# Kernel optimization log

Hardware: AMD Instinct MI355X
Metric: run time of the kernel (lower is better)

## Reference

```python
import jax, jax.numpy as jnp
import numpy as np

N_LAYERS = 12
N_CH = 256
N_IN = 4
KS = 3
SPECT_CH = 640


def conv1d(x, w, b, dilation):
    # x: [B, T, Cin], w: [K, Cin, Cout] (WIO), SAME padding, given dilation
    y = jax.lax.conv_general_dilated(
        x, w, window_strides=(1,), padding='SAME',
        rhs_dilation=(dilation,), dimension_numbers=('NWC', 'WIO', 'NWC'))
    return y + b


def setup_inputs() -> dict:
    key = jax.random.key(0)
    ks = jax.random.split(key, 16)
    s = 0.02
    inp = {}
    inp['audio'] = jax.random.normal(ks[0], (8, 4096, N_IN), dtype=jnp.float32)
    inp['spect'] = jax.random.normal(ks[1], (8, 4096, SPECT_CH), dtype=jnp.float32)
    # start 1x1 conv: [Cin, Cout]
    inp['w_start'] = jax.random.normal(ks[2], (N_IN, N_CH), dtype=jnp.float32) * s
    inp['b_start'] = jnp.zeros((N_CH,), dtype=jnp.float32)
    # dilated in_layers: stacked [L, K, Cin, 2*Cout]
    inp['w_in'] = jax.random.normal(ks[3], (N_LAYERS, KS, N_CH, 2 * N_CH), dtype=jnp.float32) * s
    inp['b_in'] = jnp.zeros((N_LAYERS, 2 * N_CH), dtype=jnp.float32)
    # cond 1x1 convs: stacked [L, SPECT_CH, 2*Cout]
    inp['w_cond'] = jax.random.normal(ks[4], (N_LAYERS, SPECT_CH, 2 * N_CH), dtype=jnp.float32) * s
    inp['b_cond'] = jnp.zeros((N_LAYERS, 2 * N_CH), dtype=jnp.float32)
    # res_skip 1x1 convs: first L-1 have 2*Cout, last has Cout
    inp['w_res'] = jax.random.normal(ks[5], (N_LAYERS - 1, N_CH, 2 * N_CH), dtype=jnp.float32) * s
    inp['b_res'] = jnp.zeros((N_LAYERS - 1, 2 * N_CH), dtype=jnp.float32)
    inp['w_res_last'] = jax.random.normal(ks[6], (N_CH, N_CH), dtype=jnp.float32) * s
    inp['b_res_last'] = jnp.zeros((N_CH,), dtype=jnp.float32)
    # end 1x1 conv (zero-initialized in the original; use small random for a
    # non-degenerate numerical baseline)
    inp['w_end'] = jax.random.normal(ks[7], (N_CH, 2 * N_IN), dtype=jnp.float32) * s
    inp['b_end'] = jnp.zeros((2 * N_IN,), dtype=jnp.float32)
    return inp


def reference(audio, spect, w_start, b_start, w_in, b_in, w_cond, b_cond,
              w_res, b_res, w_res_last, b_res_last, w_end, b_end):
    # start: 1x1 conv == matmul over channels
    started = jnp.einsum('btc,cd->btd', audio, w_start) + b_start  # [B,T,256]
    # precompute all conditioning projections: [L,B,T,512]
    cond_all = jnp.einsum('btc,lcd->lbtd', spect, w_cond) + b_cond[:, None, None, :]
    output = None
    for i in range(N_LAYERS):
        in_l = conv1d(started, w_in[i], b_in[i], 2 ** i)  # [B,T,512]
        acts = in_l + cond_all[i]
        half_tanh = jnp.tanh(acts[..., :N_CH])
        half_sig = jax.nn.sigmoid(acts[..., N_CH:])
        activated = half_tanh * half_sig  # [B,T,256]
        if i < N_LAYERS - 1:
            rs = jnp.einsum('btc,cd->btd', activated, w_res[i]) + b_res[i]
            started = started + rs[..., :N_CH]
            skip = rs[..., N_CH:]
        else:
            skip = jnp.einsum('btc,cd->btd', activated, w_res_last) + b_res_last
        output = skip if output is None else output + skip
    out = jnp.einsum('btc,cd->btd', output, w_end) + b_end  # [B,T,2*N_IN]
    return out
```

## Files before the change

kernel.cpp:

```cpp
#include <hip/hip_runtime.h>
#include <cstdint>

#define PAD 2048
#define KG 1408

typedef float f32x4 __attribute__((ext_vector_type(4)));
typedef __bf16 bf16x8 __attribute__((ext_vector_type(8)));
typedef __bf16 bf16x4 __attribute__((ext_vector_type(4)));

__device__ __forceinline__ void g2l16(const void* g, void* l) {
    __builtin_amdgcn_global_load_lds(
        (__attribute__((address_space(1))) void*)(uintptr_t)g,
        (__attribute__((address_space(3))) void*)(uint32_t)(uintptr_t)l,
        16, 0, 0);
}


__global__ void cvt_bf16_kernel(const float4* __restrict__ src, bf16x4* __restrict__ dst, int n4) {
    int idx = blockIdx.x * 256 + threadIdx.x;
    if (idx < n4) {
        float4 v = src[idx];
        bf16x4 o = {(__bf16)v.x, (__bf16)v.y, (__bf16)v.z, (__bf16)v.w};
        dst[idx] = o;
    }
}

__global__ void init_started_kernel(const float* __restrict__ audio, const float* __restrict__ w_start,
                                    const float* __restrict__ b_start, __bf16* __restrict__ started_pad) {
    int pr = blockIdx.x * 4 + (threadIdx.x >> 6);
    int c0 = (threadIdx.x & 63) * 4;
    int off = pr & 8191;
    bf16x4 o = {(__bf16)0.f, (__bf16)0.f, (__bf16)0.f, (__bf16)0.f};
    if (off >= PAD && off < PAD + 4096) {
        int r = ((pr >> 13) << 12) + (off - PAD);
        float a0 = audio[r * 4 + 0], a1 = audio[r * 4 + 1], a2 = audio[r * 4 + 2], a3 = audio[r * 4 + 3];
        for (int j = 0; j < 4; ++j) {
            int c = c0 + j;
            o[j] = (__bf16)(b_start[c] + a0 * w_start[c] + a1 * w_start[256 + c]
                            + a2 * w_start[512 + c] + a3 * w_start[768 + c]);
        }
    }
    *(bf16x4*)&started_pad[(size_t)pr * 256 + c0] = o;
}

__global__ void transpose_gate(const float* __restrict__ w_in, const float* __restrict__ w_cond,
                               __bf16* __restrict__ Wg) {
    __shared__ float tile[64][65];
    int i = blockIdx.z;
    int k0 = blockIdx.y * 64, n0 = blockIdx.x * 64;
    int tid = threadIdx.x, c = tid & 63, rr = tid >> 6;
    for (int it = 0; it < 16; ++it) {
        int kl = it * 4 + rr;
        int k = k0 + kl;
        int np = n0 + c;
        int phys = ((np >> 4) & 1) * 256 + (np >> 5) * 16 + (np & 15);
        float v;
        if (k < 768) v = w_in[((i * 3 + (k >> 8)) * 256 + (k & 255)) * 512 + phys];
        else         v = w_cond[(i * 640 + (k - 768)) * 512 + phys];
        tile[kl][c] = v;
    }
    __syncthreads();
    for (int it = 0; it < 16; ++it) {
        int nl = it * 4 + rr;
        Wg[(size_t)(i * 512 + n0 + nl) * KG + k0 + c] = (__bf16)tile[c][nl];
    }
}

__global__ void transpose_kn(const float* __restrict__ src, __bf16* __restrict__ dst,
                             int K, int N, int srcLS, int dstLS) {
    __shared__ float tile[64][65];
    int i = blockIdx.z;
    int k0 = blockIdx.y * 64, n0 = blockIdx.x * 64;
    int tid = threadIdx.x, c = tid & 63, rr = tid >> 6;
    const float* s = src + (size_t)i * srcLS;
    __bf16* dp = dst + (size_t)i * dstLS;
    for (int it = 0; it < 16; ++it) {
        int kl = it * 4 + rr;
        tile[kl][c] = s[(k0 + kl) * N + n0 + c];
    }
    __syncthreads();
    for (int it = 0; it < 16; ++it) {
        int nl = it * 4 + rr;
        dp[(size_t)(n0 + nl) * K + k0 + c] = (__bf16)tile[c][nl];
    }
}

__global__ void bias_gate_kernel(const float* __restrict__ b_in, const float* __restrict__ b_cond,
                                 float* __restrict__ bias) {
    int idx = blockIdx.x * 256 + threadIdx.x;
    int i = idx >> 9, np = idx & 511;
    int phys = ((np >> 4) & 1) * 256 + (np >> 5) * 16 + (np & 15);
    bias[idx] = b_in[i * 512 + phys] + b_cond[i * 512 + phys];
}

__global__ void wfold_kernel(const float* __restrict__ w_res, const float* __restrict__ w_res_last,
                             const float* __restrict__ w_end, const float* __restrict__ b_res,
                             const float* __restrict__ b_res_last, const float* __restrict__ b_end,
                             float* __restrict__ wfold, float* __restrict__ outconst) {
    if (blockIdx.x == 96) {
        __shared__ float red[256][8];
        int j = threadIdx.x;
        float bsum = b_res_last[j];
        for (int i = 0; i < 11; ++i) bsum += b_res[i * 512 + 256 + j];
        for (int c = 0; c < 8; ++c) red[j][c] = bsum * w_end[j * 8 + c];
        __syncthreads();
        if (j < 8) {
            float s = b_end[j];
            for (int t = 0; t < 256; ++t) s += red[t][j];
            outconst[j] = s;
        }
        return;
    }
    int idx = blockIdx.x * 256 + threadIdx.x;
    int i = idx >> 11, rem = idx & 2047, k = rem >> 3, c = rem & 7;
    float s = 0.f;
    if (i < 11) {
        const float* wr = w_res + (size_t)(i * 256 + k) * 512 + 256;
        for (int j = 0; j < 256; ++j) s += wr[j] * w_end[j * 8 + c];
    } else {
        const float* wr = w_res_last + k * 256;
        for (int j = 0; j < 256; ++j) s += wr[j] * w_end[j * 8 + c];
    }
    wfold[idx] = s;
}


__global__ __launch_bounds__(256, 2) void gate_kernel(
    const __bf16* __restrict__ started_pad, const __bf16* __restrict__ spect,
    const __bf16* __restrict__ Wg,
    const float* __restrict__ bias,
    __bf16* __restrict__ activated, int d) {
    __shared__ __align__(16) __bf16 SMEM[24576];
    const int tid = threadIdx.x;
    const int m0 = blockIdx.x * 128;
    const int n0 = blockIdx.y * 256;
    const int padbase = ((m0 >> 12) << 13) + PAD + (m0 & 4095);
    const int srow = tid >> 2;
    const int skq = (tid & 3) * 8;
    const int wave = tid >> 6, lane = tid & 63;
    const int wm = (wave >> 1) * 64, wn = (wave & 1) * 128;
    const int quad = lane >> 4, l15 = lane & 15;

    f32x4 acc[4][8];
    for (int i = 0; i < 4; i++)
        for (int j = 0; j < 8; j++) acc[i][j] = f32x4{0.f, 0.f, 0.f, 0.f};

    const __bf16* Bbase = Wg + (n0 + srow) * KG + skq;

    bf16x8 rA[2], rB[4];
    auto loadTile = [&](int kk) {
        const __bf16* gA0;
        int rstride;
        if (kk < 768) {
            int tap = kk >> 8;
            int koff = kk & 255;
            gA0 = started_pad + (padbase + srow + (tap - 1) * d) * 256 + koff + skq;
            rstride = 256;
        } else {
            gA0 = spect + (m0 + srow) * 640 + (kk - 768) + skq;
            rstride = 640;
        }
        rA[0] = *(const bf16x8*)gA0;
        rA[1] = *(const bf16x8*)(gA0 + 64 * rstride);
        const __bf16* gB0 = Bbase + kk;
        rB[0] = *(const bf16x8*)gB0;
        rB[1] = *(const bf16x8*)(gB0 + 64 * KG);
        rB[2] = *(const bf16x8*)(gB0 + 128 * KG);
        rB[3] = *(const bf16x8*)(gB0 + 192 * KG);
    };
    auto stash = [&](int buf) {
        __bf16* Ab = SMEM + buf * 4096;
        __bf16* Bb = SMEM + 8192 + buf * 8192;
        *(bf16x8*)&Ab[srow * 32 + skq] = rA[0];
        *(bf16x8*)&Ab[(64 + srow) * 32 + skq] = rA[1];
        *(bf16x8*)&Bb[srow * 32 + skq] = rB[0];
        *(bf16x8*)&Bb[(64 + srow) * 32 + skq] = rB[1];
        *(bf16x8*)&Bb[(128 + srow) * 32 + skq] = rB[2];
        *(bf16x8*)&Bb[(192 + srow) * 32 + skq] = rB[3];
    };

    loadTile(0);
    stash(0);
    loadTile(32);
    __syncthreads();

    for (int ks = 0; ks < 44; ++ks) {
        const int cur = ks & 1, nxt = cur ^ 1;
        const __bf16* Ab = SMEM + cur * 4096;
        const __bf16* Bb = SMEM + 8192 + cur * 8192;
        bf16x8 a[4], b[8];
        for (int mi = 0; mi < 4; mi++) a[mi] = *(const bf16x8*)&Ab[(wm + mi * 16 + l15) * 32 + quad * 8];
        for (int ni = 0; ni < 8; ni++) b[ni] = *(const bf16x8*)&Bb[(wn + ni * 16 + l15) * 32 + quad * 8];
        if (ks + 1 < 44) stash(nxt);
        if (ks + 2 < 44) loadTile((ks + 2) * 32);
        for (int mi = 0; mi < 4; mi++)
            for (int ni = 0; ni < 8; ni++)
                acc[mi][ni] = __builtin_amdgcn_mfma_f32_16x16x32_bf16(a[mi], b[ni], acc[mi][ni], 0, 0, 0);
        __syncthreads();
    }

    __bf16* tile = SMEM;
    for (int nj = 0; nj < 4; ++nj) {
        int colT = wn + nj * 32 + l15;
        float bt = bias[n0 + colT];
        float bs = bias[n0 + colT + 16];
        int chl = (wn >> 1) + nj * 16 + l15;
        for (int mi = 0; mi < 4; ++mi) {
            for (int reg = 0; reg < 4; ++reg) {
                int row = wm + mi * 16 + quad * 4 + reg;
                float xt = acc[mi][2 * nj][reg] + bt;
                float xs = acc[mi][2 * nj + 1][reg] + bs;
                float th = 2.f / (1.f + __expf(-2.f * xt)) - 1.f;
                float sg = 1.f / (1.f + __expf(-xs));
                tile[row * 132 + chl] = (__bf16)(th * sg);
            }
        }
    }
    __syncthreads();
    int chb = n0 >> 1;
    for (int pass = 0; pass < 8; ++pass) {
        int row = (tid >> 4) + 16 * pass;
        int seg = tid & 15;
        bf16x8 v = *(const bf16x8*)&tile[row * 132 + seg * 8];
        *(bf16x8*)&activated[(m0 + row) * 256 + chb + seg * 8] = v;
    }
}

__global__ __launch_bounds__(256) void res_kernel(
    const __bf16* __restrict__ activated, const __bf16* __restrict__ Wr,
    const float* __restrict__ b_res,
    const float* __restrict__ wfold,
    const float* __restrict__ outconst,
    __bf16* __restrict__ started_pad, float* __restrict__ out, int initOut) {
    __shared__ __align__(16) __bf16 As[128 * 32];
    __shared__ __align__(16) __bf16 Bs[128 * 32];
    __shared__ __align__(16) __bf16 WfB[16 * 264];
    const int tid = threadIdx.x;
    const int m0 = blockIdx.x * 128;
    const int n0 = blockIdx.y * 128;
    const int srow = tid >> 2;
    const int skq = (tid & 3) * 8;
    const int wave = tid >> 6, lane = tid & 63;
    const int wm = (wave >> 1) * 64, wn = (wave & 1) * 64;
    const int quad = lane >> 4, l15 = lane & 15;
    const bool doOut = (blockIdx.y == 0);
    const bool outWave = doOut && (wn == 0);

    f32x4 acc[4][4];
    for (int i = 0; i < 4; i++)
        for (int j = 0; j < 4; j++) acc[i][j] = f32x4{0.f, 0.f, 0.f, 0.f};
    f32x4 acc_o[4];
    for (int i = 0; i < 4; i++) acc_o[i] = f32x4{0.f, 0.f, 0.f, 0.f};

    const __bf16* Abase = activated + (m0 + srow) * 256 + skq;
    const __bf16* Bbase = Wr + (n0 + srow) * 256 + skq;

    if (doOut) {
        for (int t = 0; t < 16; ++t) {
            int e = t * 256 + tid;
            int col = e >> 8, k = e & 255;
            WfB[col * 264 + k] = (col < 8) ? (__bf16)wfold[k * 8 + col] : (__bf16)0.f;
        }
    }

    for (int ks = 0; ks < 8; ++ks) {
        int kk = ks * 32;
        g2l16(Abase + kk, &As[srow * 32 + skq]);
        g2l16(Abase + kk + 64 * 256, &As[(64 + srow) * 32 + skq]);
        g2l16(Bbase + kk, &Bs[srow * 32 + skq]);
        g2l16(Bbase + kk + 64 * 256, &Bs[(64 + srow) * 32 + skq]);
        __syncthreads();
        bf16x8 a[4], b[4];
        for (int mi = 0; mi < 4; mi++) a[mi] = *(const bf16x8*)&As[(wm + mi * 16 + l15) * 32 + quad * 8];
        for (int ni = 0; ni < 4; ni++) b[ni] = *(const bf16x8*)&Bs[(wn + ni * 16 + l15) * 32 + quad * 8];
        for (int mi = 0; mi < 4; mi++)
            for (int ni = 0; ni < 4; ni++)
                acc[mi][ni] = __builtin_amdgcn_mfma_f32_16x16x32_bf16(a[mi], b[ni], acc[mi][ni], 0, 0, 0);
        if (outWave) {
            bf16x8 bx = *(const bf16x8*)&WfB[l15 * 264 + kk + quad * 8];
            for (int mi = 0; mi < 4; mi++)
                acc_o[mi] = __builtin_amdgcn_mfma_f32_16x16x32_bf16(a[mi], bx, acc_o[mi], 0, 0, 0);
        }
        __syncthreads();
    }

    for (int ni = 0; ni < 4; ++ni) {
        int col = n0 + wn + ni * 16 + l15;
        float bcol = b_res[col];
        for (int mi = 0; mi < 4; ++mi) {
            for (int reg = 0; reg < 4; ++reg) {
                int r = m0 + wm + mi * 16 + quad * 4 + reg;
                int pr = ((r >> 12) << 13) + PAD + (r & 4095);
                int idx = pr * 256 + col;
                float f = (float)started_pad[idx] + acc[mi][ni][reg] + bcol;
                started_pad[idx] = (__bf16)f;
            }
        }
    }
    if (outWave && l15 < 8) {
        for (int mi = 0; mi < 4; ++mi) {
            for (int reg = 0; reg < 4; ++reg) {
                int r = m0 + wm + mi * 16 + quad * 4 + reg;
                float base = initOut ? outconst[l15] : out[r * 8 + l15];
                out[r * 8 + l15] = base + acc_o[mi][reg];
            }
        }
    }
}

__global__ __launch_bounds__(256) void outacc_kernel(
    const __bf16* __restrict__ activated, const float* __restrict__ wfold,
    float* __restrict__ out) {
    __shared__ __align__(16) float Wf[2048];
    int tid = threadIdx.x;
    ((float4*)Wf)[tid] = ((const float4*)wfold)[tid];
    ((float4*)Wf)[256 + tid] = ((const float4*)wfold)[256 + tid];
    __syncthreads();
    int row2 = tid >> 1, half = tid & 1;
    int r = blockIdx.x * 128 + row2;
    const bf16x8* ap = (const bf16x8*)(activated + r * 256);
    const float4* wf = (const float4*)Wf;
    float ox = 0.f, oy = 0.f, oz = 0.f, ow = 0.f;
    for (int c8 = 0; c8 < 32; ++c8) {
        bf16x8 av = ap[c8];
        for (int e = 0; e < 8; ++e) {
            float a = (float)av[e];
            float4 w = wf[(c8 * 8 + e) * 2 + half];
            ox += a * w.x; oy += a * w.y; oz += a * w.z; ow += a * w.w;
        }
    }
    float4* op = (float4*)&out[r * 8 + half * 4];
    float4 o = *op;
    o.x += ox; o.y += oy; o.z += oz; o.w += ow;
    *op = o;
}


extern "C" void kernel_launch(void* const* d_in, const int* in_sizes, int n_in,
                              void* d_out, int out_size, void* d_ws, size_t ws_size,
                              hipStream_t stream) {
    const float* audio      = (const float*)d_in[0];
    const float* spect      = (const float*)d_in[1];
    const float* w_start    = (const float*)d_in[2];
    const float* b_start    = (const float*)d_in[3];
    const float* w_in       = (const float*)d_in[4];
    const float* b_in       = (const float*)d_in[5];
    const float* w_cond     = (const float*)d_in[6];
    const float* b_cond     = (const float*)d_in[7];
    const float* w_res      = (const float*)d_in[8];
    const float* b_res      = (const float*)d_in[9];
    const float* w_res_last = (const float*)d_in[10];
    const float* b_res_last = (const float*)d_in[11];
    const float* w_end      = (const float*)d_in[12];
    const float* b_end      = (const float*)d_in[13];
    float* out = (float*)d_out;

    char* ws = (char*)d_ws;
    __bf16* started_pad = (__bf16*)ws; ws += 33554432;
    __bf16* activated   = (__bf16*)ws; ws += 16777216;
    __bf16* spect_bf    = (__bf16*)ws; ws += 41943040;
    __bf16* Wg          = (__bf16*)ws; ws += 17301504;
    __bf16* Wr          = (__bf16*)ws; ws += 1441792;
    float*  wfold       = (float*)ws;  ws += 98304;
    float*  biasg       = (float*)ws;  ws += 24576;
    float*  outconst    = (float*)ws;  ws += 256;

    init_started_kernel<<<dim3(16384), 256, 0, stream>>>(audio, w_start, b_start, started_pad);
    cvt_bf16_kernel<<<dim3(20480), 256, 0, stream>>>((const float4*)spect, (bf16x4*)spect_bf, 5242880);
    transpose_gate<<<dim3(8, 22, 12), 256, 0, stream>>>(w_in, w_cond, Wg);
    transpose_kn<<<dim3(4, 4, 11), 256, 0, stream>>>(w_res, Wr, 256, 512, 256 * 512, 256 * 256);
    bias_gate_kernel<<<dim3(24), 256, 0, stream>>>(b_in, b_cond, biasg);
    wfold_kernel<<<dim3(97), 256, 0, stream>>>(w_res, w_res_last, w_end, b_res, b_res_last, b_end,
                                               wfold, outconst);

    for (int i = 0; i < 12; ++i) {
        gate_kernel<<<dim3(256, 2), 256, 0, stream>>>(
            started_pad, spect_bf, Wg + (size_t)i * 512 * KG, biasg + i * 512, activated, 1 << i);
        if (i < 11) {
            res_kernel<<<dim3(256, 2), 256, 0, stream>>>(
                activated, Wr + (size_t)i * 256 * 256, b_res + i * 512,
                wfold + i * 2048, outconst, started_pad, out, i == 0 ? 1 : 0);
        } else {
            outacc_kernel<<<dim3(256), 256, 0, stream>>>(activated, wfold + 11 * 2048, out);
        }
    }
}
```

Measured before the change: 1.106 ms.

## Use direct global-to-LDS loads with XOR-swizzled LDS layout in gate and res GEMMs

Result: no change. 1.096 ms (-0.9%).

```diff
diff --git a/kernel.cpp b/kernel.cpp
--- a/kernel.cpp
+++ b/kernel.cpp
@@ -135,77 +135,79 @@
     const int m0 = blockIdx.x * 128;
     const int n0 = blockIdx.y * 256;
     const int padbase = ((m0 >> 12) << 13) + PAD + (m0 & 4095);
-    const int srow = tid >> 2;
-    const int skq = (tid & 3) * 8;
     const int wave = tid >> 6, lane = tid & 63;
     const int wm = (wave >> 1) * 64, wn = (wave & 1) * 128;
     const int quad = lane >> 4, l15 = lane & 15;
 
+    const int srow = tid >> 2;
+    const int swcol = ((tid & 3) ^ (srow & 3)) * 8;
+
     f32x4 acc[4][8];
+    #pragma unroll
     for (int i = 0; i < 4; i++)
+        #pragma unroll
         for (int j = 0; j < 8; j++) acc[i][j] = f32x4{0.f, 0.f, 0.f, 0.f};
 
-    const __bf16* Bbase = Wg + (n0 + srow) * KG + skq;
-
-    bf16x8 rA[2], rB[4];
-    auto loadTile = [&](int kk) {
-        const __bf16* gA0;
-        int rstride;
+    auto stage = [&](int kk, int s) {
+        __bf16* Ad = SMEM + s * 4096 + tid * 8;
+        const __bf16* gA;
+        int rs;
         if (kk < 768) {
             int tap = kk >> 8;
             int koff = kk & 255;
-            gA0 = started_pad + (padbase + srow + (tap - 1) * d) * 256 + koff + skq;
-            rstride = 256;
+            gA = started_pad + (size_t)(padbase + srow + (tap - 1) * d) * 256 + koff + swcol;
+            rs = 256;
         } else {
-            gA0 = spect + (m0 + srow) * 640 + (kk - 768) + skq;
-            rstride = 640;
-        }
-        rA[0] = *(const bf16x8*)gA0;
-        rA[1] = *(const bf16x8*)(gA0 + 64 * rstride);
-        const __bf16* gB0 = Bbase + kk;
-        rB[0] = *(const bf16x8*)gB0;
-        rB[1] = *(const bf16x8*)(gB0 + 64 * KG);
-        rB[2] = *(const bf16x8*)(gB0 + 128 * KG);
-        rB[3] = *(const bf16x8*)(gB0 + 192 * KG);
+            gA = spect + (size_t)(m0 + srow) * 640 + (kk - 768) + swcol;
+            rs = 640;
+        }
+        g2l16(gA, Ad);
+        g2l16(gA + 64 * rs, Ad + 2048);
+        const __bf16* gB = Wg + (size_t)(n0 + srow) * KG + kk + swcol;
+        __bf16* Bd = SMEM + 8192 + s * 8192 + tid * 8;
+        g2l16(gB, Bd);
+        g2l16(gB + 64 * KG, Bd + 2048);
+        g2l16(gB + 128 * KG, Bd + 4096);
+        g2l16(gB + 192 * KG, Bd + 6144);
     };
-    auto stash = [&](int buf) {
-        __bf16* Ab = SMEM + buf * 4096;
-        __bf16* Bb = SMEM + 8192 + buf * 8192;
-        *(bf16x8*)&Ab[srow * 32 + skq] = rA[0];
-        *(bf16x8*)&Ab[(64 + srow) * 32 + skq] = rA[1];
-        *(bf16x8*)&Bb[srow * 32 + skq] = rB[0];
-        *(bf16x8*)&Bb[(64 + srow) * 32 + skq] = rB[1];
-        *(bf16x8*)&Bb[(128 + srow) * 32 + skq] = rB[2];
-        *(bf16x8*)&Bb[(192 + srow) * 32 + skq] = rB[3];
-    };
-
-    loadTile(0);
-    stash(0);
-    loadTile(32);
+
+    stage(0, 0);
     __syncthreads();
 
     for (int ks = 0; ks < 44; ++ks) {
-        const int cur = ks & 1, nxt = cur ^ 1;
-        const __bf16* Ab = SMEM + cur * 4096;
-        const __bf16* Bb = SMEM + 8192 + cur * 8192;
+        const int cur = ks & 1;
+        if (ks + 1 < 44) stage((ks + 1) * 32, cur ^ 1);
+        const __bf16* As = SMEM + cur * 4096;
+        const __bf16* Bs = SMEM + 8192 + cur * 8192;
         bf16x8 a[4], b[8];
-        for (int mi = 0; mi < 4; mi++) a[mi] = *(const bf16x8*)&Ab[(wm + mi * 16 + l15) * 32 + quad * 8];
-        for (int ni = 0; ni < 8; ni++) b[ni] = *(const bf16x8*)&Bb[(wn + ni * 16 + l15) * 32 + quad * 8];
-        if (ks + 1 < 44) stash(nxt);
-        if (ks + 2 < 44) loadTile((ks + 2) * 32);
+        #pragma unroll
+        for (int mi = 0; mi < 4; mi++) {
+            int row = wm + mi * 16 + l15;
+            a[mi] = *(const bf16x8*)&As[row * 32 + ((quad ^ (row & 3)) * 8)];
+        }
+        #pragma unroll
+        for (int ni = 0; ni < 8; ni++) {
+            int row = wn + ni * 16 + l15;
+            b[ni] = *(const bf16x8*)&Bs[row * 32 + ((quad ^ (row & 3)) * 8)];
+        }
+        #pragma unroll
         for (int mi = 0; mi < 4; mi++)
+            #pragma unroll
             for (int ni = 0; ni < 8; ni++)
                 acc[mi][ni] = __builtin_amdgcn_mfma_f32_16x16x32_bf16(a[mi], b[ni], acc[mi][ni], 0, 0, 0);
         __syncthreads();
     }
 
     __bf16* tile = SMEM;
+    #pragma unroll
     for (int nj = 0; nj < 4; ++nj) {
         int colT = wn + nj * 32 + l15;
         float bt = bias[n0 + colT];
         float bs = bias[n0 + colT + 16];
         int chl = (wn >> 1) + nj * 16 + l15;
+        #pragma unroll
         for (int mi = 0; mi < 4; ++mi) {
+            #pragma unroll
             for (int reg = 0; reg < 4; ++reg) {
                 int row = wm + mi * 16 + quad * 4 + reg;
                 float xt = acc[mi][2 * nj][reg] + bt;
@@ -239,7 +241,7 @@
     const int m0 = blockIdx.x * 128;
     const int n0 = blockIdx.y * 128;
     const int srow = tid >> 2;
-    const int skq = (tid & 3) * 8;
+    const int swcol = ((tid & 3) ^ (srow & 3)) * 8;
     const int wave = tid >> 6, lane = tid & 63;
     const int wm = (wave >> 1) * 64, wn = (wave & 1) * 64;
     const int quad = lane >> 4, l15 = lane & 15;
@@ -252,8 +254,8 @@
     f32x4 acc_o[4];
     for (int i = 0; i < 4; i++) acc_o[i] = f32x4{0.f, 0.f, 0.f, 0.f};
 
-    const __bf16* Abase = activated + (m0 + srow) * 256 + skq;
-    const __bf16* Bbase = Wr + (n0 + srow) * 256 + skq;
+    const __bf16* Abase = activated + (m0 + srow) * 256 + swcol;
+    const __bf16* Bbase = Wr + (n0 + srow) * 256 + swcol;
 
     if (doOut) {
         for (int t = 0; t < 16; ++t) {
@@ -265,14 +267,20 @@
 
     for (int ks = 0; ks < 8; ++ks) {
         int kk = ks * 32;
-        g2l16(Abase + kk, &As[srow * 32 + skq]);
-        g2l16(Abase + kk + 64 * 256, &As[(64 + srow) * 32 + skq]);
-        g2l16(Bbase + kk, &Bs[srow * 32 + skq]);
-        g2l16(Bbase + kk + 64 * 256, &Bs[(64 + srow) * 32 + skq]);
+        g2l16(Abase + kk, &As[tid * 8]);
+        g2l16(Abase + kk + 64 * 256, &As[tid * 8 + 2048]);
+        g2l16(Bbase + kk, &Bs[tid * 8]);
+        g2l16(Bbase + kk + 64 * 256, &Bs[tid * 8 + 2048]);
         __syncthreads();
         bf16x8 a[4], b[4];
-        for (int mi = 0; mi < 4; mi++) a[mi] = *(const bf16x8*)&As[(wm + mi * 16 + l15) * 32 + quad * 8];
-        for (int ni = 0; ni < 4; ni++) b[ni] = *(const bf16x8*)&Bs[(wn + ni * 16 + l15) * 32 + quad * 8];
+        for (int mi = 0; mi < 4; mi++) {
+            int row = wm + mi * 16 + l15;
+            a[mi] = *(const bf16x8*)&As[row * 32 + ((quad ^ (row & 3)) * 8)];
+        }
+        for (int ni = 0; ni < 4; ni++) {
+            int row = wn + ni * 16 + l15;
+            b[ni] = *(const bf16x8*)&Bs[row * 32 + ((quad ^ (row & 3)) * 8)];
+        }
         for (int mi = 0; mi < 4; mi++)
             for (int ni = 0; ni < 4; ni++)
                 acc[mi][ni] = __builtin_amdgcn_mfma_f32_16x16x32_bf16(a[mi], b[ni], acc[mi][ni], 0, 0, 0);
```
